# Kernel tuning notes

Hardware: AMD Instinct MI355X
Metric: run time of the kernel (lower is better)

Reference implementation:

```python
import jax, jax.numpy as jnp
import numpy as np

B, D, N_TYPES = 512, 768, 16
MARGIN = 1.0


def setup_inputs() -> dict:
    key = jax.random.key(0)
    k1, k2 = jax.random.split(key)
    entity_types = jax.random.randint(k1, (B,), 0, N_TYPES, dtype=jnp.int64)
    embeddings = jax.random.normal(k2, (B, D), dtype=jnp.float32)
    return {"entity_types": entity_types, "embeddings": embeddings}


def _pairwise_l2(x):
    # Euclidean distance matrix [B, B], matching torch.cdist(x, x, p=2)
    sq_norm = jnp.sum(x * x, axis=-1)  # [B]
    sq = sq_norm[:, None] + sq_norm[None, :] - 2.0 * (x @ x.T)
    sq = jnp.maximum(sq, 0.0)
    # safe sqrt: zero gradient where sq == 0 (diagonal)
    return jnp.where(sq > 0, jnp.sqrt(jnp.where(sq > 0, sq, 1.0)), 0.0)


def reference(entity_types, embeddings):
    # type_coherence[i, j] = (type_i == type_j)
    type_coherence = entity_types[:, None] == entity_types[None, :]  # [B, B]
    # valid_triplets[a, p, n] = same_type(a, p) & different_type(a, n)
    valid_triplets = type_coherence[:, :, None] & (~type_coherence)[:, None, :]  # [B, B, B]
    distances = _pairwise_l2(embeddings)  # [B, B]
    # triplet_distances[a, p, n] = (d[a, p] - d[a, n]) masked by validity
    triplet_distances = (distances[:, :, None] - distances[:, None, :]) * valid_triplets
    # NOTE: faithful to original — margin added to ALL B^3 entries before clamp,
    # so each invalid triplet contributes clamp(margin, 0) = margin to the sum.
    loss = jnp.sum(jnp.maximum(triplet_distances + MARGIN, 0.0))
    return loss / jnp.sum(valid_triplets)
```

## Files before the change

### kernel.cpp

```cpp
#include <hip/hip_runtime.h>
#include <hip/hip_bf16.h>

#define BSZ 512
#define DIM 768
#define KSPLIT 4
#define KSEG (DIM / KSPLIT)
#define TILE 64
#define NTYPES 16
#define MARGIN 1.0f
#define LDSPITCH (KSEG + 8)

typedef short bf16x8 __attribute__((ext_vector_type(8)));
typedef float f32x4 __attribute__((ext_vector_type(4)));

__global__ __launch_bounds__(256) void dot_partial_kernel(
    const float* __restrict__ emb,
    float* __restrict__ part,
    float* __restrict__ ndiag,
    float* __restrict__ out)
{
    const int tid = threadIdx.x;
    const int blk = blockIdx.x;
    const int ks = blk >> 6;
    const int tile = blk & 63;
    const int ti = tile >> 3, tj = tile & 7;
    const int i0 = ti * TILE, j0 = tj * TILE;

    if (blk == 0 && tid == 0) out[0] = 0.f;

    __shared__ ushort sA[TILE][LDSPITCH];
    __shared__ ushort sB[TILE][LDSPITCH];

    #pragma unroll
    for (int it = 0; it < 24; ++it) {
        const int flat = it * 256 + tid;
        const int row = flat / 48;
        const int c4 = flat - row * 48;
        const int grow = (row < TILE) ? (i0 + row) : (j0 + row - TILE);
        const float4 v = *(const float4*)(emb + (size_t)grow * DIM + ks * KSEG + c4 * 4);
        __hip_bfloat162 h0 = __float22bfloat162_rn(make_float2(v.x, v.y));
        __hip_bfloat162 h1 = __float22bfloat162_rn(make_float2(v.z, v.w));
        unsigned u0, u1;
        __builtin_memcpy(&u0, &h0, 4);
        __builtin_memcpy(&u1, &h1, 4);
        ushort* dst = (row < TILE) ? &sA[row][c4 * 4] : &sB[row - TILE][c4 * 4];
        *(uint2*)dst = make_uint2(u0, u1);
    }
    __syncthreads();

    const int lane = tid & 63;
    const int w = tid >> 6;
    const int m = lane & 15;
    const int q = lane >> 4;

    f32x4 acc0 = {0.f, 0.f, 0.f, 0.f};
    f32x4 acc1 = {0.f, 0.f, 0.f, 0.f};
    f32x4 acc2 = {0.f, 0.f, 0.f, 0.f};
    f32x4 acc3 = {0.f, 0.f, 0.f, 0.f};

    const ushort* arow = &sA[w * 16 + m][q * 8];
    const ushort* b0r = &sB[0 * 16 + m][q * 8];
    const ushort* b1r = &sB[1 * 16 + m][q * 8];
    const ushort* b2r = &sB[2 * 16 + m][q * 8];
    const ushort* b3r = &sB[3 * 16 + m][q * 8];

    #pragma unroll
    for (int kc = 0; kc < KSEG / 32; ++kc) {
        const bf16x8 af = *(const bf16x8*)(arow + kc * 32);
        const bf16x8 bf0 = *(const bf16x8*)(b0r + kc * 32);
        const bf16x8 bf1 = *(const bf16x8*)(b1r + kc * 32);
        const bf16x8 bf2 = *(const bf16x8*)(b2r + kc * 32);
        const bf16x8 bf3 = *(const bf16x8*)(b3r + kc * 32);
        acc0 = __builtin_amdgcn_mfma_f32_16x16x32_bf16(af, bf0, acc0, 0, 0, 0);
        acc1 = __builtin_amdgcn_mfma_f32_16x16x32_bf16(af, bf1, acc1, 0, 0, 0);
        acc2 = __builtin_amdgcn_mfma_f32_16x16x32_bf16(af, bf2, acc2, 0, 0, 0);
        acc3 = __builtin_amdgcn_mfma_f32_16x16x32_bf16(af, bf3, acc3, 0, 0, 0);
    }

    float* pbuf = part + (size_t)ks * BSZ * BSZ;
    const int gi = i0 + w * 16 + 4 * q;
    #pragma unroll
    for (int r = 0; r < 4; ++r) {
        float* prow = pbuf + (size_t)(gi + r) * BSZ + j0;
        prow[0 * 16 + m] = acc0[r];
        prow[1 * 16 + m] = acc1[r];
        prow[2 * 16 + m] = acc2[r];
        prow[3 * 16 + m] = acc3[r];
    }
    if (ti == tj && (m >> 2) == q) {
        const f32x4 accw = (w == 0) ? acc0 : (w == 1) ? acc1 : (w == 2) ? acc2 : acc3;
        ndiag[ks * BSZ + i0 + w * 16 + m] = accw[m & 3];
    }
}

__global__ __launch_bounds__(256) void triplet_kernel(
    const float* __restrict__ part, const float* __restrict__ ndiag,
    const int* __restrict__ types, float* __restrict__ out)
{
    const int a = blockIdx.x;
    const int tid = threadIdx.x;
    const int lane = tid & 63;
    __shared__ float nrm[BSZ];
    __shared__ float pos[BSZ], neg[BSZ];
    __shared__ int npos, nneg;
    __shared__ float wsum[4];
    __shared__ int cnt[NTYPES];
    if (tid == 0) { npos = 0; nneg = 0; }
    if (tid < NTYPES) cnt[tid] = 0;
    for (int j = tid; j < BSZ; j += 256)
        nrm[j] = ndiag[j] + ndiag[BSZ + j] + ndiag[2 * BSZ + j] + ndiag[3 * BSZ + j];
    const int ta = types[a];
    __syncthreads();

    const float na = nrm[a];
    const size_t rb = (size_t)a * BSZ;
    const size_t PS = (size_t)BSZ * BSZ;

    for (int j = tid; j < BSZ; j += 256) {
        const int tj = types[j];
        atomicAdd(&cnt[tj], 1);
        const float sp = part[rb + j] + part[PS + rb + j]
                       + part[2 * PS + rb + j] + part[3 * PS + rb + j];
        const float d = sqrtf(fmaxf(na + nrm[j] - 2.f * sp, 0.f));
        const bool isp = (tj == ta);
        const unsigned long long mm = __ballot(isp);
        const unsigned long long below = mm & ((1ull << lane) - 1ull);
        const int cp = __popcll(mm);
        int basep = 0, basen = 0;
        if (lane == 0) {
            basep = atomicAdd(&npos, cp);
            basen = atomicAdd(&nneg, 64 - cp);
        }
        basep = __shfl(basep, 0);
        basen = __shfl(basen, 0);
        const int pbelow = (int)__popcll(below);
        if (isp) pos[basep + pbelow] = d;
        else     neg[basen + (lane - pbelow)] = d;
    }
    __syncthreads();
    const int np = npos, nn = nneg;

    float local = 0.f;
    for (int pi = 0; pi < np; ++pi) {
        const float dpm = pos[pi] + MARGIN;
        for (int n = tid; n < nn; n += 256)
            local += fmaxf(dpm - neg[n], 0.f);
    }

    #pragma unroll
    for (int off = 32; off > 0; off >>= 1) local += __shfl_down(local, off);
    if (lane == 0) wsum[tid >> 6] = local;
    __syncthreads();
    if (tid == 0) {
        long long V = 0;
        #pragma unroll
        for (int t = 0; t < NTYPES; ++t) {
            long long c = cnt[t];
            V += c * c * (long long)(BSZ - c);
        }
        double blocksum = (double)wsum[0] + (double)wsum[1]
                        + (double)wsum[2] + (double)wsum[3];
        float contrib = (float)(blocksum / (double)V);
        if (a == 0) {
            const long long B3 = (long long)BSZ * BSZ * BSZ;
            contrib += (float)((double)(B3 - V) * (double)MARGIN / (double)V);
        }
        atomicAdd(out, contrib);
    }
}

extern "C" void kernel_launch(void* const* d_in, const int* in_sizes, int n_in,
                              void* d_out, int out_size, void* d_ws, size_t ws_size,
                              hipStream_t stream) {
    const int* types = (const int*)d_in[0];
    const float* emb = (const float*)d_in[1];
    float* out = (float*)d_out;

    float* part = (float*)d_ws;
    float* ndiag = part + (size_t)KSPLIT * BSZ * BSZ;

    dot_partial_kernel<<<256, 256, 0, stream>>>(emb, part, ndiag, out);
    triplet_kernel<<<BSZ, 256, 0, stream>>>(part, ndiag, types, out);
}
```

Measured before the change: 73.67 us.

## Compute full-K 32x32 distance tiles with fp32 norms, drop K-split partials

The Gram kernel no longer splits K into four partial buffers. Each block computes a full-depth 32x32 tile, works out fp32 row norms while converting to bf16, and writes the final sqrt distance directly. This removes the 4x partial-sum traffic and the norm/distance reconstruction from the triplet kernel, which now reads one value per pair. In exchange each block does a longer serial MFMA chain with one accumulator per wave, and the diagonal is forced to zero explicitly.

```diff
diff --git a/kernel.cpp b/kernel.cpp
--- a/kernel.cpp
+++ b/kernel.cpp
@@ -3,125 +3,105 @@
 
 #define BSZ 512
 #define DIM 768
-#define KSPLIT 4
-#define KSEG (DIM / KSPLIT)
-#define TILE 64
 #define NTYPES 16
 #define MARGIN 1.0f
-#define LDSPITCH (KSEG + 8)
+#define PITCH (DIM + 8)
 
 typedef short bf16x8 __attribute__((ext_vector_type(8)));
 typedef float f32x4 __attribute__((ext_vector_type(4)));
 
-__global__ __launch_bounds__(256) void dot_partial_kernel(
+__global__ __launch_bounds__(256) void dist_kernel(
     const float* __restrict__ emb,
-    float* __restrict__ part,
-    float* __restrict__ ndiag,
+    float* __restrict__ dist,
     float* __restrict__ out)
 {
     const int tid = threadIdx.x;
     const int blk = blockIdx.x;
-    const int ks = blk >> 6;
-    const int tile = blk & 63;
-    const int ti = tile >> 3, tj = tile & 7;
-    const int i0 = ti * TILE, j0 = tj * TILE;
+    const int ti = blk >> 4, tj = blk & 15;
+    const int i0 = ti * 32, j0 = tj * 32;
 
     if (blk == 0 && tid == 0) out[0] = 0.f;
 
-    __shared__ ushort sA[TILE][LDSPITCH];
-    __shared__ ushort sB[TILE][LDSPITCH];
+    __shared__ ushort sE[64][PITCH];
+    __shared__ float nrm64[64];
 
-    #pragma unroll
-    for (int it = 0; it < 24; ++it) {
-        const int flat = it * 256 + tid;
-        const int row = flat / 48;
-        const int c4 = flat - row * 48;
-        const int grow = (row < TILE) ? (i0 + row) : (j0 + row - TILE);
-        const float4 v = *(const float4*)(emb + (size_t)grow * DIM + ks * KSEG + c4 * 4);
-        __hip_bfloat162 h0 = __float22bfloat162_rn(make_float2(v.x, v.y));
-        __hip_bfloat162 h1 = __float22bfloat162_rn(make_float2(v.z, v.w));
-        unsigned u0, u1;
-        __builtin_memcpy(&u0, &h0, 4);
-        __builtin_memcpy(&u1, &h1, 4);
-        ushort* dst = (row < TILE) ? &sA[row][c4 * 4] : &sB[row - TILE][c4 * 4];
-        *(uint2*)dst = make_uint2(u0, u1);
+    {
+        const int row = tid >> 2;
+        const int qq = tid & 3;
+        const int grow = (row < 32) ? (i0 + row) : (j0 + row - 32);
+        const float* gsrc = emb + (size_t)grow * DIM;
+        float np = 0.f;
+        #pragma unroll
+        for (int i = 0; i < 48; ++i) {
+            const int c4 = qq * 48 + i;
+            const float4 v = *(const float4*)(gsrc + c4 * 4);
+            np = fmaf(v.x, v.x, np); np = fmaf(v.y, v.y, np);
+            np = fmaf(v.z, v.z, np); np = fmaf(v.w, v.w, np);
+            __hip_bfloat162 h0 = __float22bfloat162_rn(make_float2(v.x, v.y));
+            __hip_bfloat162 h1 = __float22bfloat162_rn(make_float2(v.z, v.w));
+            unsigned u0, u1;
+            __builtin_memcpy(&u0, &h0, 4);
+            __builtin_memcpy(&u1, &h1, 4);
+            *(uint2*)&sE[row][c4 * 4] = make_uint2(u0, u1);
+        }
+        np += __shfl_xor(np, 1);
+        np += __shfl_xor(np, 2);
+        if (qq == 0) nrm64[row] = np;
     }
     __syncthreads();
 
     const int lane = tid & 63;
     const int w = tid >> 6;
+    const int wr = w >> 1, wc = w & 1;
     const int m = lane & 15;
     const int q = lane >> 4;
 
-    f32x4 acc0 = {0.f, 0.f, 0.f, 0.f};
-    f32x4 acc1 = {0.f, 0.f, 0.f, 0.f};
-    f32x4 acc2 = {0.f, 0.f, 0.f, 0.f};
-    f32x4 acc3 = {0.f, 0.f, 0.f, 0.f};
+    const ushort* arow = &sE[wr * 16 + m][q * 8];
+    const ushort* brow = &sE[32 + wc * 16 + m][q * 8];
 
-    const ushort* arow = &sA[w * 16 + m][q * 8];
-    const ushort* b0r = &sB[0 * 16 + m][q * 8];
-    const ushort* b1r = &sB[1 * 16 + m][q * 8];
-    const ushort* b2r = &sB[2 * 16 + m][q * 8];
-    const ushort* b3r = &sB[3 * 16 + m][q * 8];
-
+    f32x4 acc = {0.f, 0.f, 0.f, 0.f};
     #pragma unroll
-    for (int kc = 0; kc < KSEG / 32; ++kc) {
+    for (int kc = 0; kc < DIM / 32; ++kc) {
         const bf16x8 af = *(const bf16x8*)(arow + kc * 32);
-        const bf16x8 bf0 = *(const bf16x8*)(b0r + kc * 32);
-        const bf16x8 bf1 = *(const bf16x8*)(b1r + kc * 32);
-        const bf16x8 bf2 = *(const bf16x8*)(b2r + kc * 32);
-        const bf16x8 bf3 = *(const bf16x8*)(b3r + kc * 32);
-        acc0 = __builtin_amdgcn_mfma_f32_16x16x32_bf16(af, bf0, acc0, 0, 0, 0);
-        acc1 = __builtin_amdgcn_mfma_f32_16x16x32_bf16(af, bf1, acc1, 0, 0, 0);
-        acc2 = __builtin_amdgcn_mfma_f32_16x16x32_bf16(af, bf2, acc2, 0, 0, 0);
-        acc3 = __builtin_amdgcn_mfma_f32_16x16x32_bf16(af, bf3, acc3, 0, 0, 0);
+        const bf16x8 bf = *(const bf16x8*)(brow + kc * 32);
+        acc = __builtin_amdgcn_mfma_f32_16x16x32_bf16(af, bf, acc, 0, 0, 0);
     }
 
-    float* pbuf = part + (size_t)ks * BSZ * BSZ;
-    const int gi = i0 + w * 16 + 4 * q;
+    const float nb = nrm64[32 + wc * 16 + m];
+    const int gcol = j0 + wc * 16 + m;
     #pragma unroll
     for (int r = 0; r < 4; ++r) {
-        float* prow = pbuf + (size_t)(gi + r) * BSZ + j0;
-        prow[0 * 16 + m] = acc0[r];
-        prow[1 * 16 + m] = acc1[r];
-        prow[2 * 16 + m] = acc2[r];
-        prow[3 * 16 + m] = acc3[r];
-    }
-    if (ti == tj && (m >> 2) == q) {
-        const f32x4 accw = (w == 0) ? acc0 : (w == 1) ? acc1 : (w == 2) ? acc2 : acc3;
-        ndiag[ks * BSZ + i0 + w * 16 + m] = accw[m & 3];
+        const int lrow = wr * 16 + 4 * q + r;
+        const int grow = i0 + lrow;
+        const float na = nrm64[lrow];
+        float d = sqrtf(fmaxf(na + nb - 2.f * acc[r], 0.f));
+        if (grow == gcol) d = 0.f;
+        dist[(size_t)grow * BSZ + gcol] = d;
     }
 }
 
 __global__ __launch_bounds__(256) void triplet_kernel(
-    const float* __restrict__ part, const float* __restrict__ ndiag,
-    const int* __restrict__ types, float* __restrict__ out)
+    const float* __restrict__ dist, const int* __restrict__ types,
+    float* __restrict__ out)
 {
     const int a = blockIdx.x;
     const int tid = threadIdx.x;
     const int lane = tid & 63;
-    __shared__ float nrm[BSZ];
     __shared__ float pos[BSZ], neg[BSZ];
     __shared__ int npos, nneg;
     __shared__ float wsum[4];
     __shared__ int cnt[NTYPES];
     if (tid == 0) { npos = 0; nneg = 0; }
     if (tid < NTYPES) cnt[tid] = 0;
-    for (int j = tid; j < BSZ; j += 256)
-        nrm[j] = ndiag[j] + ndiag[BSZ + j] + ndiag[2 * BSZ + j] + ndiag[3 * BSZ + j];
     const int ta = types[a];
     __syncthreads();
 
-    const float na = nrm[a];
     const size_t rb = (size_t)a * BSZ;
-    const size_t PS = (size_t)BSZ * BSZ;
 
     for (int j = tid; j < BSZ; j += 256) {
         const int tj = types[j];
         atomicAdd(&cnt[tj], 1);
-        const float sp = part[rb + j] + part[PS + rb + j]
-                       + part[2 * PS + rb + j] + part[3 * PS + rb + j];
-        const float d = sqrtf(fmaxf(na + nrm[j] - 2.f * sp, 0.f));
+        const float d = dist[rb + j];
         const bool isp = (tj == ta);
         const unsigned long long mm = __ballot(isp);
         const unsigned long long below = mm & ((1ull << lane) - 1ull);
@@ -176,9 +156,8 @@
     const float* emb = (const float*)d_in[1];
     float* out = (float*)d_out;
 
-    float* part = (float*)d_ws;
-    float* ndiag = part + (size_t)KSPLIT * BSZ * BSZ;
+    float* dist = (float*)d_ws;
 
-    dot_partial_kernel<<<256, 256, 0, stream>>>(emb, part, ndiag, out);
-    triplet_kernel<<<BSZ, 256, 0, stream>>>(part, ndiag, types, out);
+    dist_kernel<<<256, 256, 0, stream>>>(emb, dist, out);
+    triplet_kernel<<<BSZ, 256, 0, stream>>>(dist, types, out);
 }
```

After: 76.28 us. 3.5% more time.
